# Kernel tuning notes

Measured on AMD Instinct MI355X. Metric: run time of the kernel, lower is better.

## Reference

```python
import jax, jax.numpy as jnp
import numpy as np

B, N, C, CS, CP, H, L = 1, 2048, 128, 128, 16, 4, 3
NQ, NK = 32, 128  # local attention window: n_queries, n_keys
EPS = 1e-5


def _make_beta(n):
    l = np.arange(n)[:, None]
    m = np.arange(n)[None, :]
    con = np.zeros((n, n), dtype=bool)
    for c in np.arange(NQ / 2, n, NQ):
        con |= (np.abs(l - c) < NQ / 2) & (np.abs(m - c) < NK / 2)
    return np.where(con, 0.0, -1e10).astype(np.float32)


def setup_inputs() -> dict:
    key = jax.random.key(0)
    ks = iter(jax.random.split(key, 32))
    w = lambda *shape: jax.random.normal(next(ks), shape, dtype=jnp.float32) * 0.02
    inp = {
        'a': jax.random.normal(next(ks), (B, N, C), dtype=jnp.float32),
        's': jax.random.normal(next(ks), (B, N, CS), dtype=jnp.float32),
        'z': jax.random.normal(next(ks), (B, N, N, CP), dtype=jnp.float32),
        'beta': jnp.asarray(_make_beta(N))[None],
        'ada1_ln_w': jnp.ones((L, CS)), 'ada1_lin_w': w(L, CS, C),
        'ada1_lin_b': jnp.zeros((L, C)), 'ada1_nb_w': w(L, CS, C),
        'lnz_w': jnp.ones((L, CP)), 'lnz_b': jnp.zeros((L, CP)),
        'zinj_w': w(L, CP, H),
        'q_w': w(L, C, C), 'q_b': jnp.zeros((L, C)),
        'k_w': w(L, C, C), 'v_w': w(L, C, C),
        'g_w': w(L, C, C), 'o_w': w(L, C, C),
        'agate_w': w(L, CS, C), 'agate_b': jnp.full((L, C), -2.0),
        'ada2_ln_w': jnp.ones((L, CS)), 'ada2_lin_w': w(L, CS, C),
        'ada2_lin_b': jnp.zeros((L, C)), 'ada2_nb_w': w(L, CS, C),
        'lin1_w': w(L, C, 2 * C), 'lin2_w': w(L, C, 2 * C), 'lin3_w': w(L, 2 * C, C),
        'tgate_w': w(L, CS, C), 'tgate_b': jnp.full((L, C), -2.0),
    }
    return inp


def _ln(x):
    mu = jnp.mean(x, axis=-1, keepdims=True)
    var = jnp.var(x, axis=-1, keepdims=True)
    return (x - mu) * jax.lax.rsqrt(var + EPS)


def _adaln(a, s, ln_w, lin_w, lin_b, nb_w):
    # AdaLN: LN(a) gated & shifted by LN(s)
    a = _ln(a)
    sn = _ln(s) * ln_w
    return jax.nn.sigmoid(sn @ lin_w + lin_b) * a + sn @ nb_w


def _forward(a, s, z, beta, ada1_ln_w, ada1_lin_w, ada1_lin_b, ada1_nb_w,
             lnz_w, lnz_b, zinj_w, q_w, q_b, k_w, v_w, g_w, o_w,
             agate_w, agate_b, ada2_ln_w, ada2_lin_w, ada2_lin_b, ada2_nb_w,
             lin1_w, lin2_w, lin3_w, tgate_w, tgate_b):
    b_, n_, c_ = a.shape
    h_ = zinj_w.shape[-1]
    d_ = c_ // h_
    scale = 1.0 / np.sqrt(d_).astype(np.float32)
    zn0 = _ln(z)  # shared pre-affine LN of pair rep
    for i in range(q_w.shape[0]):
        # --- AttentionPairBias ---
        ah = _adaln(a, s, ada1_ln_w[i], ada1_lin_w[i], ada1_lin_b[i], ada1_nb_w[i])
        zb = jnp.einsum('bijc,ch->bhij', zn0 * lnz_w[i] + lnz_b[i], zinj_w[i])
        q = ((ah @ q_w[i] + q_b[i]) * scale).reshape(b_, n_, h_, d_)
        k = (ah @ k_w[i]).reshape(b_, n_, h_, d_)
        v = (ah @ v_w[i]).reshape(b_, n_, h_, d_)
        scores = jnp.einsum('bihd,bjhd->bhij', q, k) + zb + beta[:, None]
        p = jax.nn.softmax(scores, axis=-1)
        o = jnp.einsum('bhij,bjhd->bihd', p, v).reshape(b_, n_, c_)
        o = o * jax.nn.sigmoid(ah @ g_w[i])
        attn = (o @ o_w[i]) * jax.nn.sigmoid(s @ agate_w[i] + agate_b[i])
        # --- ConditionedTransitionBlock ---
        th = _adaln(a, s, ada2_ln_w[i], ada2_lin_w[i], ada2_lin_b[i], ada2_nb_w[i])
        bb = jax.nn.silu(th @ lin1_w[i]) * (th @ lin2_w[i])
        trans = jax.nn.sigmoid(s @ tgate_w[i] + tgate_b[i]) * th * (bb @ lin3_w[i])
        a = attn + trans
    return a


def reference(a, s, z, beta, ada1_ln_w, ada1_lin_w, ada1_lin_b, ada1_nb_w,
              lnz_w, lnz_b, zinj_w, q_w, q_b, k_w, v_w, g_w, o_w,
              agate_w, agate_b, ada2_ln_w, ada2_lin_w, ada2_lin_b, ada2_nb_w,
              lin1_w, lin2_w, lin3_w, tgate_w, tgate_b):
    return _forward(a, s, z, beta, ada1_ln_w, ada1_lin_w, ada1_lin_b, ada1_nb_w,
                    lnz_w, lnz_b, zinj_w, q_w, q_b, k_w, v_w, g_w, o_w,
                    agate_w, agate_b, ada2_ln_w, ada2_lin_w, ada2_lin_b, ada2_nb_w,
                    lin1_w, lin2_w, lin3_w, tgate_w, tgate_b)
```

## Files before the change

### kernel.cpp

```cpp
#include <hip/hip_runtime.h>


#define NT 2048

__device__ __forceinline__ float sig_(float x) { return 1.0f / (1.0f + __expf(-x)); }

__device__ __forceinline__ float redsum32(float v) {
#pragma unroll
  for (int o = 16; o > 0; o >>= 1) v += __shfl_xor(v, o);
  return v;
}

__device__ __forceinline__ void mm4(const float* __restrict__ W, int ldw,
                                    const float* As_row, int K, int c0, float* acc) {
  const float* __restrict__ wp = W + c0;
  for (int k = 0; k < K; k += 4) {
    float4 a4 = *(const float4*)(As_row + k);
#pragma unroll
    for (int kk = 0; kk < 4; ++kk) {
      float a = ((const float*)&a4)[kk];
      float4 w0 = *(const float4*)(wp);
      acc[0] = fmaf(a, w0.x, acc[0]);
      acc[1] = fmaf(a, w0.y, acc[1]);
      acc[2] = fmaf(a, w0.z, acc[2]);
      acc[3] = fmaf(a, w0.w, acc[3]);
      wp += ldw;
    }
  }
}

__device__ __forceinline__ void mm4x2(const float* __restrict__ W1,
                                      const float* __restrict__ W2, int ldw,
                                      const float* As_row, int K, int c0,
                                      float* acc1, float* acc2) {
  const float* __restrict__ wp1 = W1 + c0;
  const float* __restrict__ wp2 = W2 + c0;
  for (int k = 0; k < K; k += 4) {
    float4 a4 = *(const float4*)(As_row + k);
#pragma unroll
    for (int kk = 0; kk < 4; ++kk) {
      float a = ((const float*)&a4)[kk];
      float4 w0 = *(const float4*)(wp1);
      float4 u0 = *(const float4*)(wp2);
      acc1[0] = fmaf(a, w0.x, acc1[0]);
      acc1[1] = fmaf(a, w0.y, acc1[1]);
      acc1[2] = fmaf(a, w0.z, acc1[2]);
      acc1[3] = fmaf(a, w0.w, acc1[3]);
      acc2[0] = fmaf(a, u0.x, acc2[0]);
      acc2[1] = fmaf(a, u0.y, acc2[1]);
      acc2[2] = fmaf(a, u0.z, acc2[2]);
      acc2[3] = fmaf(a, u0.w, acc2[3]);
      wp1 += ldw; wp2 += ldw;
    }
  }
}

__global__ __launch_bounds__(256) void k_ln_rows(const float* __restrict__ X,
                                                 float* __restrict__ Y) {
  int row  = blockIdx.x * 4 + (threadIdx.x >> 6);
  int lane = threadIdx.x & 63;
  const float* xr = X + (size_t)row * 128;
  float x0 = xr[lane], x1 = xr[lane + 64];
  float s = x0 + x1;
#pragma unroll
  for (int o = 32; o > 0; o >>= 1) s += __shfl_xor(s, o);
  float mu = s * (1.0f / 128.0f);
  float d0 = x0 - mu, d1 = x1 - mu;
  float v = d0 * d0 + d1 * d1;
#pragma unroll
  for (int o = 32; o > 0; o >>= 1) v += __shfl_xor(v, o);
  float rs = rsqrtf(v * (1.0f / 128.0f) + 1e-5f);
  float* yr = Y + (size_t)row * 128;
  yr[lane] = d0 * rs;
  yr[lane + 64] = d1 * rs;
}

__global__ __launch_bounds__(256) void k_gates(
    const float* __restrict__ s, const float* __restrict__ agw,
    const float* __restrict__ agb, const float* __restrict__ tgw,
    const float* __restrict__ tgb, float* __restrict__ gatesA,
    float* __restrict__ gatesT) {
  __shared__ float As[8 * 132];
  int r0 = blockIdx.x * 8;
  int bz = blockIdx.y;
  int l = bz % 3, which = bz / 3;
  const float* W = (which ? tgw : agw) + (size_t)l * 128 * 128;
  const float* bias = (which ? tgb : agb) + (size_t)l * 128;
  float* outp = (which ? gatesT : gatesA) + (size_t)l * NT * 128;
  int tid = threadIdx.x;
  int r = tid >> 5, sub = tid & 31;
  *(float4*)&As[r * 132 + sub * 4] =
      *(const float4*)(s + (size_t)(r0 + r) * 128 + sub * 4);
  __syncthreads();
  int c0 = sub << 2;
  float acc[4] = {0, 0, 0, 0};
  mm4(W, 128, &As[r * 132], 128, c0, acc);
  size_t base = (size_t)(r0 + r) * 128 + c0;
#pragma unroll
  for (int j = 0; j < 4; ++j) outp[base + j] = sig_(acc[j] + bias[c0 + j]);
}

__global__ __launch_bounds__(256) void k_adaln12(
    const float* __restrict__ a, const float* __restrict__ ln_s,
    const float* __restrict__ lnw1, const float* __restrict__ linw1,
    const float* __restrict__ linb1, const float* __restrict__ nbw1,
    const float* __restrict__ lnw2, const float* __restrict__ linw2,
    const float* __restrict__ linb2, const float* __restrict__ nbw2,
    float* __restrict__ ah, float* __restrict__ th) {
  __shared__ float Sn[8 * 132];
  __shared__ float La[8 * 132];
  int r0 = blockIdx.x * 8;
  int y = blockIdx.y;
  const float* lnw  = y ? lnw2 : lnw1;
  const float* linw = y ? linw2 : linw1;
  const float* linb = y ? linb2 : linb1;
  const float* nbw  = y ? nbw2 : nbw1;
  float* outp = y ? th : ah;
  int tid = threadIdx.x;
  int r = tid >> 5, sub = tid & 31;
  {
    float4 v = *(const float4*)(ln_s + (size_t)(r0 + r) * 128 + sub * 4);
    float4 sc = *(const float4*)(lnw + sub * 4);
    v.x *= sc.x; v.y *= sc.y; v.z *= sc.z; v.w *= sc.w;
    *(float4*)&Sn[r * 132 + sub * 4] = v;
  }
  {
    float4 x = *(const float4*)(a + (size_t)(r0 + r) * 128 + sub * 4);
    float s = redsum32(x.x + x.y + x.z + x.w);
    float mu = s * (1.0f / 128.0f);
    float4 d = make_float4(x.x - mu, x.y - mu, x.z - mu, x.w - mu);
    float v = redsum32(d.x * d.x + d.y * d.y + d.z * d.z + d.w * d.w);
    float rs = rsqrtf(v * (1.0f / 128.0f) + 1e-5f);
    d.x *= rs; d.y *= rs; d.z *= rs; d.w *= rs;
    *(float4*)&La[r * 132 + sub * 4] = d;
  }
  __syncthreads();
  int c0 = sub << 2;
  float acc1[4] = {0, 0, 0, 0}, acc2[4] = {0, 0, 0, 0};
  mm4x2(linw, nbw, 128, &Sn[r * 132], 128, c0, acc1, acc2);
  size_t base = (size_t)(r0 + r) * 128 + c0;
#pragma unroll
  for (int j = 0; j < 4; ++j) {
    float g = sig_(acc1[j] + linb[c0 + j]);
    outp[base + j] = g * La[r * 132 + c0 + j] + acc2[j];
  }
}

__global__ __launch_bounds__(256) void k_qkvg(
    const float* __restrict__ ah, const float* __restrict__ qw,
    const float* __restrict__ kw, const float* __restrict__ vw,
    const float* __restrict__ gw, const float* __restrict__ qb,
    float* __restrict__ qkvg) {
  __shared__ float As[8 * 132];
  int r0 = blockIdx.x * 8;
  int mat = blockIdx.y;
  const float* W = (mat == 0) ? qw : (mat == 1) ? kw : (mat == 2) ? vw : gw;
  int tid = threadIdx.x;
  int r = tid >> 5, sub = tid & 31;
  *(float4*)&As[r * 132 + sub * 4] =
      *(const float4*)(ah + (size_t)(r0 + r) * 128 + sub * 4);
  __syncthreads();
  int c0 = sub << 2;
  float acc[4] = {0, 0, 0, 0};
  mm4(W, 128, &As[r * 132], 128, c0, acc);
  float* op = qkvg + (size_t)(r0 + r) * 512 + mat * 128 + c0;
  if (mat == 0) {
#pragma unroll
    for (int j = 0; j < 4; ++j)
      op[j] = (acc[j] + qb[c0 + j]) * 0.17677669529663687f;
  } else if (mat == 3) {
#pragma unroll
    for (int j = 0; j < 4; ++j) op[j] = sig_(acc[j]);
  } else {
#pragma unroll
    for (int j = 0; j < 4; ++j) op[j] = acc[j];
  }
}

__global__ __launch_bounds__(256) void k_wattn(
    const float* __restrict__ qkvg, const float* __restrict__ z,
    const float* __restrict__ lnzw, const float* __restrict__ lnzb,
    const float* __restrict__ zinj, float* __restrict__ og,
    float* __restrict__ colpart) {
  __shared__ float Qs[8][128];
  __shared__ float S[8][4][132];
  __shared__ float KV[32][128];
  __shared__ float wz[4][16];
  __shared__ float bzw[2][4];
  __shared__ float red[2][128];

  const int tid = threadIdx.x;
  const int bx = blockIdx.x;
  if (bx >= 256) {
    int b = bx - 256;
    int rr = tid >> 7, c = tid & 127;
    float acc = 0.0f;
    for (int t = 0; t < 16; ++t) {
      int row = b * 32 + rr + t * 2;
      acc += qkvg[(size_t)row * 512 + 256 + c];
    }
    red[rr][c] = acc;
    __syncthreads();
    if (rr == 0) colpart[b * 128 + c] = red[0][c] + red[1][c];
    return;
  }

  const int win = bx >> 2, sub4 = bx & 3;
  const int cen = 16 + 32 * win;
  const int i0 = cen - 15 + 8 * sub4;
  const int nrows = (sub4 == 3) ? 7 : 8;
  const int jlo = max(0, cen - 63), jhi = min(2047, cen + 63);
  const int nk = jhi - jlo + 1;

  if (tid < 64) {
    int h = tid & 3, c = tid >> 2;
    wz[h][c] = lnzw[c] * zinj[c * 4 + h];
  }
  if (tid < 8) {
    int h = tid & 3, which = tid >> 2;
    float acc = 0.0f;
    for (int c = 0; c < 16; ++c) acc += (which ? lnzb[c] : lnzw[c]) * zinj[c * 4 + h];
    bzw[which][h] = acc;
  }
  {
    int r = tid >> 5, sub = tid & 31;
    int i = i0 + min(r, nrows - 1);
    *(float4*)&Qs[r][sub * 4] = *(const float4*)(qkvg + (size_t)i * 512 + sub * 4);
  }
  __syncthreads();

  for (int idx = tid; idx < 8 * 128; idx += 256) {
    int r = idx >> 7, jj = idx & 127;
    if (jj < nk) {
      int i = i0 + min(r, nrows - 1);
      int j = jlo + jj;
      const float* zp = z + ((size_t)i * 2048 + j) * 16;
      float x[16];
      *(float4*)&x[0]  = *(const float4*)(zp + 0);
      *(float4*)&x[4]  = *(const float4*)(zp + 4);
      *(float4*)&x[8]  = *(const float4*)(zp + 8);
      *(float4*)&x[12] = *(const float4*)(zp + 12);
      float sm = 0.0f;
#pragma unroll
      for (int c = 0; c < 16; ++c) sm += x[c];
      float mu = sm * (1.0f / 16.0f);
      float var = 0.0f;
#pragma unroll
      for (int c = 0; c < 16; ++c) { float d = x[c] - mu; var = fmaf(d, d, var); }
      float rs = rsqrtf(var * (1.0f / 16.0f) + 1e-5f);
#pragma unroll
      for (int h = 0; h < 4; ++h) {
        float dot = 0.0f;
#pragma unroll
        for (int c = 0; c < 16; ++c) dot = fmaf(x[c], wz[h][c], dot);
        S[r][h][jj] = fmaf(rs, dot - mu * bzw[0][h], bzw[1][h]);
      }
    } else {
#pragma unroll
      for (int h = 0; h < 4; ++h) S[r][h][jj] = -1e30f;
    }
  }
  __syncthreads();

  {
    const int r = tid >> 5, h = (tid >> 3) & 3, part = tid & 7;
    float qreg[32];
#pragma unroll
    for (int d4 = 0; d4 < 32; d4 += 4)
      *(float4*)&qreg[d4] = *(const float4*)&Qs[r][h * 32 + d4];
    for (int kb = 0; kb < 128; kb += 32) {
      for (int idx = tid; idx < 32 * 32; idx += 256) {
        int kk = idx >> 5, c4 = (idx & 31) << 2;
        int j = jlo + kb + kk;
        int cs = (c4 + ((kk >> 3) << 2)) & 127;
        float4 val = make_float4(0.f, 0.f, 0.f, 0.f);
        if (j <= jhi) val = *(const float4*)(qkvg + (size_t)j * 512 + 128 + c4);
        *(float4*)&KV[kk][cs] = val;
      }
      __syncthreads();
#pragma unroll
      for (int u = 0; u < 4; ++u) {
        int jj = part + (u << 3);
        int rot = (jj >> 3) << 2;
        float dot = 0.0f;
#pragma unroll
        for (int d4 = 0; d4 < 32; d4 += 4) {
          int cs = (h * 32 + d4 + rot) & 127;
          float4 kv = *(const float4*)&KV[jj][cs];
          dot = fmaf(qreg[d4 + 0], kv.x, dot);
          dot = fmaf(qreg[d4 + 1], kv.y, dot);
          dot = fmaf(qreg[d4 + 2], kv.z, dot);
          dot = fmaf(qreg[d4 + 3], kv.w, dot);
        }
        S[r][h][kb + jj] += dot;
      }
      __syncthreads();
    }
  }

  {
    const int rh = tid >> 3, part = tid & 7;
    const int sr = rh >> 2, sh = rh & 3;
    float* Srow = &S[sr][sh][0];
    float m = -1e30f;
#pragma unroll
    for (int st = 0; st < 16; ++st) m = fmaxf(m, Srow[part + (st << 3)]);
#pragma unroll
    for (int o = 4; o > 0; o >>= 1) m = fmaxf(m, __shfl_xor(m, o));
    float ss = 0.0f;
#pragma unroll
    for (int st = 0; st < 16; ++st) {
      int jj = part + (st << 3);
      float e = __expf(Srow[jj] - m);
      Srow[jj] = e;
      ss += e;
    }
#pragma unroll
    for (int o = 4; o > 0; o >>= 1) ss += __shfl_xor(ss, o);
    float inv = 1.0f / ss;
#pragma unroll
    for (int st = 0; st < 16; ++st) Srow[part + (st << 3)] *= inv;
  }
  __syncthreads();

  {
    const int r = tid >> 5, cg = tid & 31;
    const int ca = cg << 2;
    const int h = cg >> 3;
    float acc[4] = {0, 0, 0, 0};
    for (int kb = 0; kb < 128; kb += 32) {
      for (int idx = tid; idx < 32 * 32; idx += 256) {
        int kk = idx >> 5, c4 = (idx & 31) << 2;
        int j = jlo + kb + kk;
        int cs = (c4 + ((kk >> 3) << 2)) & 127;
        float4 val = make_float4(0.f, 0.f, 0.f, 0.f);
        if (j <= jhi) val = *(const float4*)(qkvg + (size_t)j * 512 + 256 + c4);
        *(float4*)&KV[kk][cs] = val;
      }
      __syncthreads();
#pragma unroll 4
      for (int kk = 0; kk < 32; ++kk) {
        int rot = (kk >> 3) << 2;
        float sa = S[r][h][kb + kk];
        float4 va = *(const float4*)&KV[kk][(ca + rot) & 127];
        acc[0] = fmaf(sa, va.x, acc[0]);
        acc[1] = fmaf(sa, va.y, acc[1]);
        acc[2] = fmaf(sa, va.z, acc[2]);
        acc[3] = fmaf(sa, va.w, acc[3]);
      }
      __syncthreads();
    }
    if (r < nrows) {
      int i = i0 + r;
      float4 ga = *(const float4*)(qkvg + (size_t)i * 512 + 384 + ca);
      float4 oa = make_float4(acc[0] * ga.x, acc[1] * ga.y, acc[2] * ga.z, acc[3] * ga.w);
      *(float4*)(og + (size_t)i * 128 + ca) = oa;
    }
  }
}

__global__ __launch_bounds__(256) void k_oproj(const float* __restrict__ og,
                                               const float* __restrict__ ow,
                                               const float* __restrict__ gA,
                                               const float* __restrict__ colpart,
                                               const float* __restrict__ qkvg,
                                               float* __restrict__ attn) {
  __shared__ float As[8 * 132];
  __shared__ float red[2][128];
  int r0 = blockIdx.x * 8;
  int tid = threadIdx.x;
  int r = tid >> 5, sub = tid & 31;
  *(float4*)&As[r * 132 + sub * 4] =
      *(const float4*)(og + (size_t)(r0 + r) * 128 + sub * 4);
  __syncthreads();
  if ((r0 & 31) == 0) {
    int col = tid & 127, half = tid >> 7;
    float acc = 0.0f;
    for (int b = half; b < 64; b += 2) acc += colpart[b * 128 + col];
    red[half][col] = acc;
    __syncthreads();
    if (half == 0) {
      float mv = (red[0][col] + red[1][col]) * (1.0f / 2048.0f);
      As[col] = mv * qkvg[(size_t)r0 * 512 + 384 + col];
    }
    __syncthreads();
  }
  int c0 = sub << 2;
  float acc[4] = {0, 0, 0, 0};
  mm4(ow, 128, &As[r * 132], 128, c0, acc);
  size_t base = (size_t)(r0 + r) * 128 + c0;
#pragma unroll
  for (int j = 0; j < 4; ++j) attn[base + j] = acc[j] * gA[base + j];
}

__global__ __launch_bounds__(256) void k_lin12(const float* __restrict__ th,
                                               const float* __restrict__ w1,
                                               const float* __restrict__ w2,
                                               float* __restrict__ bb) {
  __shared__ float As[8 * 132];
  int r0 = blockIdx.x * 8;
  int cb0 = blockIdx.y * 128;
  int tid = threadIdx.x;
  int r = tid >> 5, sub = tid & 31;
  *(float4*)&As[r * 132 + sub * 4] =
      *(const float4*)(th + (size_t)(r0 + r) * 128 + sub * 4);
  __syncthreads();
  int c0 = cb0 + (sub << 2);
  float acc1[4] = {0, 0, 0, 0}, acc2[4] = {0, 0, 0, 0};
  mm4x2(w1, w2, 256, &As[r * 132], 128, c0, acc1, acc2);
  size_t base = (size_t)(r0 + r) * 256 + c0;
#pragma unroll
  for (int j = 0; j < 4; ++j) {
    float x1 = acc1[j];
    bb[base + j] = x1 * sig_(x1) * acc2[j];
  }
}

__global__ __launch_bounds__(256) void k_lin3comb(
    const float* __restrict__ bb, const float* __restrict__ w3,
    const float* __restrict__ attn, const float* __restrict__ gT,
    const float* __restrict__ th, float* __restrict__ outp) {
  __shared__ float As[8 * 260];
  int r0 = blockIdx.x * 8;
  int tid = threadIdx.x;
  for (int idx = tid; idx < 8 * 64; idx += 256) {
    int row = idx >> 6, c4 = (idx & 63) << 2;
    *(float4*)&As[row * 260 + c4] = *(const float4*)(bb + (size_t)(r0 + row) * 256 + c4);
  }
  __syncthreads();
  int r = tid >> 5, sub = tid & 31;
  int c0 = sub << 2;
  float acc[4] = {0, 0, 0, 0};
  mm4(w3, 128, &As[r * 260], 256, c0, acc);
  size_t base = (size_t)(r0 + r) * 128 + c0;
#pragma unroll
  for (int j = 0; j < 4; ++j)
    outp[base + j] = attn[base + j] + gT[base + j] * th[base + j] * acc[j];
}

extern "C" void kernel_launch(void* const* d_in, const int* in_sizes, int n_in,
                              void* d_out, int out_size, void* d_ws, size_t ws_size,
                              hipStream_t stream) {
  (void)in_sizes; (void)n_in; (void)out_size; (void)ws_size;
  const float* A_in   = (const float*)d_in[0];
  const float* S_in   = (const float*)d_in[1];
  const float* Z_in   = (const float*)d_in[2];
  const float* ada1_ln_w  = (const float*)d_in[4];
  const float* ada1_lin_w = (const float*)d_in[5];
  const float* ada1_lin_b = (const float*)d_in[6];
  const float* ada1_nb_w  = (const float*)d_in[7];
  const float* lnz_w      = (const float*)d_in[8];
  const float* lnz_b      = (const float*)d_in[9];
  const float* zinj_w     = (const float*)d_in[10];
  const float* q_w        = (const float*)d_in[11];
  const float* q_b        = (const float*)d_in[12];
  const float* k_w        = (const float*)d_in[13];
  const float* v_w        = (const float*)d_in[14];
  const float* g_w        = (const float*)d_in[15];
  const float* o_w        = (const float*)d_in[16];
  const float* agate_w    = (const float*)d_in[17];
  const float* agate_b    = (const float*)d_in[18];
  const float* ada2_ln_w  = (const float*)d_in[19];
  const float* ada2_lin_w = (const float*)d_in[20];
  const float* ada2_lin_b = (const float*)d_in[21];
  const float* ada2_nb_w  = (const float*)d_in[22];
  const float* lin1_w     = (const float*)d_in[23];
  const float* lin2_w     = (const float*)d_in[24];
  const float* lin3_w     = (const float*)d_in[25];
  const float* tgate_w    = (const float*)d_in[26];
  const float* tgate_b    = (const float*)d_in[27];

  const int N = NT, C = 128;
  float* ws = (float*)d_ws;
  float* ln_s    = ws;
  float* ah      = ln_s + (size_t)N * C;
  float* th      = ah + (size_t)N * C;
  float* qkvg    = th + (size_t)N * C;
  float* og      = qkvg + (size_t)N * 512;
  float* attn    = og + (size_t)N * C;
  float* bb      = attn + (size_t)N * C;
  float* gatesA  = bb + (size_t)N * 256;
  float* gatesT  = gatesA + (size_t)3 * N * C;
  float* colpart = gatesT + (size_t)3 * N * C;

  dim3 blk(256);
  k_ln_rows<<<512, blk, 0, stream>>>(S_in, ln_s);
  k_gates<<<dim3(256, 6), blk, 0, stream>>>(S_in, agate_w, agate_b, tgate_w,
                                            tgate_b, gatesA, gatesT);
  const float* acur = A_in;
  for (int l = 0; l < 3; ++l) {
    k_adaln12<<<dim3(256, 2), blk, 0, stream>>>(
        acur, ln_s, ada1_ln_w + (size_t)l * C, ada1_lin_w + (size_t)l * C * C,
        ada1_lin_b + (size_t)l * C, ada1_nb_w + (size_t)l * C * C,
        ada2_ln_w + (size_t)l * C, ada2_lin_w + (size_t)l * C * C,
        ada2_lin_b + (size_t)l * C, ada2_nb_w + (size_t)l * C * C, ah, th);
    k_qkvg<<<dim3(256, 4), blk, 0, stream>>>(ah, q_w + (size_t)l * C * C,
                                             k_w + (size_t)l * C * C,
                                             v_w + (size_t)l * C * C,
                                             g_w + (size_t)l * C * C,
                                             q_b + (size_t)l * C, qkvg);
    k_lin12<<<dim3(256, 2), blk, 0, stream>>>(th, lin1_w + (size_t)l * C * 2 * C,
                                              lin2_w + (size_t)l * C * 2 * C, bb);
    k_wattn<<<320, blk, 0, stream>>>(qkvg, Z_in, lnz_w + (size_t)l * 16,
                                     lnz_b + (size_t)l * 16,
                                     zinj_w + (size_t)l * 64, og, colpart);
    k_oproj<<<256, blk, 0, stream>>>(og, o_w + (size_t)l * C * C,
                                     gatesA + (size_t)l * N * C, colpart, qkvg,
                                     attn);
    k_lin3comb<<<256, blk, 0, stream>>>(bb, lin3_w + (size_t)l * 2 * C * C, attn,
                                        gatesT + (size_t)l * N * C, th,
                                        (float*)d_out);
    acur = (const float*)d_out;
  }
}
```

Baseline: 780.6 us.

## Precompute z-bias once for all layers, prefetch K/V, fuse oproj with lin3

Adds a k_zbias kernel that reads the windowed z once and computes the layer-norm plus head projection for all three layers up front, so each layer's attention kernel loads a compact per-window bias instead of re-reading and normalising z. The attention kernel now prefetches K/V tiles into registers to overlap global loads with compute, and folds softmax normalisation into the output scaling, which removes one pass and one barrier. The output projection and lin3 combine are merged into a single tail kernel, removing the attn intermediate buffer and one launch per layer. The cost is an extra workspace buffer for the bias and more register pressure in the attention kernel.

```diff
diff --git a/kernel.cpp b/kernel.cpp
--- a/kernel.cpp
+++ b/kernel.cpp
@@ -98,6 +98,67 @@
   size_t base = (size_t)(r0 + r) * 128 + c0;
 #pragma unroll
   for (int j = 0; j < 4; ++j) outp[base + j] = sig_(acc[j] + bias[c0 + j]);
+}
+
+__global__ __launch_bounds__(256) void k_zbias(
+    const float* __restrict__ z, const float* __restrict__ lnzw,
+    const float* __restrict__ lnzb, const float* __restrict__ zinj,
+    float* __restrict__ zb) {
+  __shared__ float wz[3][4][16];
+  __shared__ float bzw[3][2][4];
+  const int tid = threadIdx.x;
+  const int bx = blockIdx.x;
+  const int win = bx >> 2, q = bx & 3;
+  const int cen = 16 + 32 * win;
+  const int i0 = cen - 15 + 8 * q;
+  const int nrows = (q == 3) ? 7 : 8;
+  const int jlo = max(0, cen - 63), jhi = min(2047, cen + 63);
+  const int nk = jhi - jlo + 1;
+  if (tid < 192) {
+    int l = tid / 64, rem = tid & 63, h = rem & 3, c = rem >> 2;
+    wz[l][h][c] = lnzw[l * 16 + c] * zinj[l * 64 + c * 4 + h];
+  }
+  if (tid < 24) {
+    int l = tid / 8, rem = tid & 7, h = rem & 3, which = rem >> 2;
+    const float* wv = (which ? lnzb : lnzw) + l * 16;
+    float acc = 0.0f;
+    for (int c = 0; c < 16; ++c) acc += wv[c] * zinj[l * 64 + c * 4 + h];
+    bzw[l][which][h] = acc;
+  }
+  __syncthreads();
+  for (int idx = tid; idx < 8 * 128; idx += 256) {
+    int r = idx >> 7, jj = idx & 127;
+    if (jj >= nk || r >= nrows) continue;
+    int i = i0 + r;
+    int j = jlo + jj;
+    const float* zp = z + ((size_t)i * 2048 + j) * 16;
+    float x[16];
+    *(float4*)&x[0]  = *(const float4*)(zp + 0);
+    *(float4*)&x[4]  = *(const float4*)(zp + 4);
+    *(float4*)&x[8]  = *(const float4*)(zp + 8);
+    *(float4*)&x[12] = *(const float4*)(zp + 12);
+    float sm = 0.0f;
+#pragma unroll
+    for (int c = 0; c < 16; ++c) sm += x[c];
+    float mu = sm * (1.0f / 16.0f);
+    float var = 0.0f;
+#pragma unroll
+    for (int c = 0; c < 16; ++c) { float d = x[c] - mu; var = fmaf(d, d, var); }
+    float rs = rsqrtf(var * (1.0f / 16.0f) + 1e-5f);
+    float* op = zb + (size_t)i * 512 + (size_t)jj * 4;
+#pragma unroll
+    for (int l = 0; l < 3; ++l) {
+      float4 o4;
+#pragma unroll
+      for (int h = 0; h < 4; ++h) {
+        float dot = 0.0f;
+#pragma unroll
+        for (int c = 0; c < 16; ++c) dot = fmaf(x[c], wz[l][h][c], dot);
+        ((float*)&o4)[h] = fmaf(rs, dot - mu * bzw[l][0][h], bzw[l][1][h]);
+      }
+      *(float4*)(op + (size_t)l * 2048 * 512) = o4;
+    }
+  }
 }
 
 __global__ __launch_bounds__(256) void k_adaln12(
@@ -178,15 +239,12 @@
 }
 
 __global__ __launch_bounds__(256) void k_wattn(
-    const float* __restrict__ qkvg, const float* __restrict__ z,
-    const float* __restrict__ lnzw, const float* __restrict__ lnzb,
-    const float* __restrict__ zinj, float* __restrict__ og,
-    float* __restrict__ colpart) {
+    const float* __restrict__ qkvg, const float* __restrict__ zb,
+    float* __restrict__ og, float* __restrict__ colpart) {
   __shared__ float Qs[8][128];
   __shared__ float S[8][4][132];
   __shared__ float KV[32][128];
-  __shared__ float wz[4][16];
-  __shared__ float bzw[2][4];
+  __shared__ float invS[8][4];
   __shared__ float red[2][128];
 
   const int tid = threadIdx.x;
@@ -212,49 +270,35 @@
   const int jlo = max(0, cen - 63), jhi = min(2047, cen + 63);
   const int nk = jhi - jlo + 1;
 
-  if (tid < 64) {
-    int h = tid & 3, c = tid >> 2;
-    wz[h][c] = lnzw[c] * zinj[c * 4 + h];
-  }
-  if (tid < 8) {
-    int h = tid & 3, which = tid >> 2;
-    float acc = 0.0f;
-    for (int c = 0; c < 16; ++c) acc += (which ? lnzb[c] : lnzw[c]) * zinj[c * 4 + h];
-    bzw[which][h] = acc;
-  }
+  int pkk[4], pc[4];
+#pragma unroll
+  for (int u = 0; u < 4; ++u) {
+    int idx = tid + u * 256;
+    pkk[u] = idx >> 5;
+    pc[u] = (idx & 31) << 2;
+  }
+  float4 pref[4];
+#pragma unroll
+  for (int u = 0; u < 4; ++u) {
+    int j = jlo + pkk[u];
+    pref[u] = (j <= jhi) ? *(const float4*)(qkvg + (size_t)j * 512 + 128 + pc[u])
+                         : make_float4(0.f, 0.f, 0.f, 0.f);
+  }
+
   {
     int r = tid >> 5, sub = tid & 31;
     int i = i0 + min(r, nrows - 1);
     *(float4*)&Qs[r][sub * 4] = *(const float4*)(qkvg + (size_t)i * 512 + sub * 4);
   }
-  __syncthreads();
-
   for (int idx = tid; idx < 8 * 128; idx += 256) {
     int r = idx >> 7, jj = idx & 127;
     if (jj < nk) {
       int i = i0 + min(r, nrows - 1);
-      int j = jlo + jj;
-      const float* zp = z + ((size_t)i * 2048 + j) * 16;
-      float x[16];
-      *(float4*)&x[0]  = *(const float4*)(zp + 0);
-      *(float4*)&x[4]  = *(const float4*)(zp + 4);
-      *(float4*)&x[8]  = *(const float4*)(zp + 8);
-      *(float4*)&x[12] = *(const float4*)(zp + 12);
-      float sm = 0.0f;
-#pragma unroll
-      for (int c = 0; c < 16; ++c) sm += x[c];
-      float mu = sm * (1.0f / 16.0f);
-      float var = 0.0f;
-#pragma unroll
-      for (int c = 0; c < 16; ++c) { float d = x[c] - mu; var = fmaf(d, d, var); }
-      float rs = rsqrtf(var * (1.0f / 16.0f) + 1e-5f);
-#pragma unroll
-      for (int h = 0; h < 4; ++h) {
-        float dot = 0.0f;
-#pragma unroll
-        for (int c = 0; c < 16; ++c) dot = fmaf(x[c], wz[h][c], dot);
-        S[r][h][jj] = fmaf(rs, dot - mu * bzw[0][h], bzw[1][h]);
-      }
+      float4 zv = *(const float4*)(zb + (size_t)i * 512 + (size_t)jj * 4);
+      S[r][0][jj] = zv.x;
+      S[r][1][jj] = zv.y;
+      S[r][2][jj] = zv.z;
+      S[r][3][jj] = zv.w;
     } else {
 #pragma unroll
       for (int h = 0; h < 4; ++h) S[r][h][jj] = -1e30f;
@@ -269,13 +313,19 @@
     for (int d4 = 0; d4 < 32; d4 += 4)
       *(float4*)&qreg[d4] = *(const float4*)&Qs[r][h * 32 + d4];
     for (int kb = 0; kb < 128; kb += 32) {
-      for (int idx = tid; idx < 32 * 32; idx += 256) {
-        int kk = idx >> 5, c4 = (idx & 31) << 2;
-        int j = jlo + kb + kk;
-        int cs = (c4 + ((kk >> 3) << 2)) & 127;
-        float4 val = make_float4(0.f, 0.f, 0.f, 0.f);
-        if (j <= jhi) val = *(const float4*)(qkvg + (size_t)j * 512 + 128 + c4);
-        *(float4*)&KV[kk][cs] = val;
+#pragma unroll
+      for (int u = 0; u < 4; ++u)
+        *(float4*)&KV[pkk[u]][(pc[u] + ((pkk[u] >> 3) << 2)) & 127] = pref[u];
+      {
+        int nxt_off = (kb < 96) ? 128 : 256;
+        int nxt_kb = (kb < 96) ? kb + 32 : 0;
+#pragma unroll
+        for (int u = 0; u < 4; ++u) {
+          int j = jlo + nxt_kb + pkk[u];
+          pref[u] = (j <= jhi)
+                        ? *(const float4*)(qkvg + (size_t)j * 512 + nxt_off + pc[u])
+                        : make_float4(0.f, 0.f, 0.f, 0.f);
+        }
       }
       __syncthreads();
 #pragma unroll
@@ -317,11 +367,8 @@
     }
 #pragma unroll
     for (int o = 4; o > 0; o >>= 1) ss += __shfl_xor(ss, o);
-    float inv = 1.0f / ss;
-#pragma unroll
-    for (int st = 0; st < 16; ++st) Srow[part + (st << 3)] *= inv;
-  }
-  __syncthreads();
+    if (part == 0) invS[sr][sh] = 1.0f / ss;
+  }
 
   {
     const int r = tid >> 5, cg = tid & 31;
@@ -329,13 +376,17 @@
     const int h = cg >> 3;
     float acc[4] = {0, 0, 0, 0};
     for (int kb = 0; kb < 128; kb += 32) {
-      for (int idx = tid; idx < 32 * 32; idx += 256) {
-        int kk = idx >> 5, c4 = (idx & 31) << 2;
-        int j = jlo + kb + kk;
-        int cs = (c4 + ((kk >> 3) << 2)) & 127;
-        float4 val = make_float4(0.f, 0.f, 0.f, 0.f);
-        if (j <= jhi) val = *(const float4*)(qkvg + (size_t)j * 512 + 256 + c4);
-        *(float4*)&KV[kk][cs] = val;
+#pragma unroll
+      for (int u = 0; u < 4; ++u)
+        *(float4*)&KV[pkk[u]][(pc[u] + ((pkk[u] >> 3) << 2)) & 127] = pref[u];
+      if (kb < 96) {
+#pragma unroll
+        for (int u = 0; u < 4; ++u) {
+          int j = jlo + kb + 32 + pkk[u];
+          pref[u] = (j <= jhi)
+                        ? *(const float4*)(qkvg + (size_t)j * 512 + 256 + pc[u])
+                        : make_float4(0.f, 0.f, 0.f, 0.f);
+        }
       }
       __syncthreads();
 #pragma unroll 4
@@ -352,45 +403,13 @@
     }
     if (r < nrows) {
       int i = i0 + r;
+      float inv = invS[r][h];
       float4 ga = *(const float4*)(qkvg + (size_t)i * 512 + 384 + ca);
-      float4 oa = make_float4(acc[0] * ga.x, acc[1] * ga.y, acc[2] * ga.z, acc[3] * ga.w);
+      float4 oa = make_float4(acc[0] * inv * ga.x, acc[1] * inv * ga.y,
+                              acc[2] * inv * ga.z, acc[3] * inv * ga.w);
       *(float4*)(og + (size_t)i * 128 + ca) = oa;
     }
   }
-}
-
-__global__ __launch_bounds__(256) void k_oproj(const float* __restrict__ og,
-                                               const float* __restrict__ ow,
-                                               const float* __restrict__ gA,
-                                               const float* __restrict__ colpart,
-                                               const float* __restrict__ qkvg,
-                                               float* __restrict__ attn) {
-  __shared__ float As[8 * 132];
-  __shared__ float red[2][128];
-  int r0 = blockIdx.x * 8;
-  int tid = threadIdx.x;
-  int r = tid >> 5, sub = tid & 31;
-  *(float4*)&As[r * 132 + sub * 4] =
-      *(const float4*)(og + (size_t)(r0 + r) * 128 + sub * 4);
-  __syncthreads();
-  if ((r0 & 31) == 0) {
-    int col = tid & 127, half = tid >> 7;
-    float acc = 0.0f;
-    for (int b = half; b < 64; b += 2) acc += colpart[b * 128 + col];
-    red[half][col] = acc;
-    __syncthreads();
-    if (half == 0) {
-      float mv = (red[0][col] + red[1][col]) * (1.0f / 2048.0f);
-      As[col] = mv * qkvg[(size_t)r0 * 512 + 384 + col];
-    }
-    __syncthreads();
-  }
-  int c0 = sub << 2;
-  float acc[4] = {0, 0, 0, 0};
-  mm4(ow, 128, &As[r * 132], 128, c0, acc);
-  size_t base = (size_t)(r0 + r) * 128 + c0;
-#pragma unroll
-  for (int j = 0; j < 4; ++j) attn[base + j] = acc[j] * gA[base + j];
 }
 
 __global__ __launch_bounds__(256) void k_lin12(const float* __restrict__ th,
@@ -416,26 +435,49 @@
   }
 }
 
-__global__ __launch_bounds__(256) void k_lin3comb(
-    const float* __restrict__ bb, const float* __restrict__ w3,
-    const float* __restrict__ attn, const float* __restrict__ gT,
+__global__ __launch_bounds__(256) void k_tail(
+    const float* __restrict__ og, const float* __restrict__ ow,
+    const float* __restrict__ gA, const float* __restrict__ colpart,
+    const float* __restrict__ qkvg, const float* __restrict__ bbuf,
+    const float* __restrict__ w3, const float* __restrict__ gT,
     const float* __restrict__ th, float* __restrict__ outp) {
-  __shared__ float As[8 * 260];
+  __shared__ float Ao[8 * 132];
+  __shared__ float Bb[8 * 260];
+  __shared__ float red[2][128];
   int r0 = blockIdx.x * 8;
   int tid = threadIdx.x;
+  int r = tid >> 5, sub = tid & 31;
+  *(float4*)&Ao[r * 132 + sub * 4] =
+      *(const float4*)(og + (size_t)(r0 + r) * 128 + sub * 4);
   for (int idx = tid; idx < 8 * 64; idx += 256) {
     int row = idx >> 6, c4 = (idx & 63) << 2;
-    *(float4*)&As[row * 260 + c4] = *(const float4*)(bb + (size_t)(r0 + row) * 256 + c4);
-  }
-  __syncthreads();
-  int r = tid >> 5, sub = tid & 31;
+    *(float4*)&Bb[row * 260 + c4] =
+        *(const float4*)(bbuf + (size_t)(r0 + row) * 256 + c4);
+  }
+  __syncthreads();
+  if ((r0 & 31) == 0) {
+    int col = tid & 127, half = tid >> 7;
+    float acc = 0.0f;
+    for (int b = half; b < 64; b += 2) acc += colpart[b * 128 + col];
+    red[half][col] = acc;
+    __syncthreads();
+    if (half == 0) {
+      float mv = (red[0][col] + red[1][col]) * (1.0f / 2048.0f);
+      Ao[col] = mv * qkvg[(size_t)r0 * 512 + 384 + col];
+    }
+    __syncthreads();
+  }
   int c0 = sub << 2;
-  float acc[4] = {0, 0, 0, 0};
-  mm4(w3, 128, &As[r * 260], 256, c0, acc);
+  float acc1[4] = {0, 0, 0, 0};
+  mm4(ow, 128, &Ao[r * 132], 128, c0, acc1);
+  float acc3[4] = {0, 0, 0, 0};
+  mm4(w3, 128, &Bb[r * 260], 256, c0, acc3);
   size_t base = (size_t)(r0 + r) * 128 + c0;
 #pragma unroll
-  for (int j = 0; j < 4; ++j)
-    outp[base + j] = attn[base + j] + gT[base + j] * th[base + j] * acc[j];
+  for (int j = 0; j < 4; ++j) {
+    float attnv = acc1[j] * gA[base + j];
+    outp[base + j] = attnv + gT[base + j] * th[base + j] * acc3[j];
+  }
 }
 
 extern "C" void kernel_launch(void* const* d_in, const int* in_sizes, int n_in,
@@ -477,16 +519,17 @@
   float* th      = ah + (size_t)N * C;
   float* qkvg    = th + (size_t)N * C;
   float* og      = qkvg + (size_t)N * 512;
-  float* attn    = og + (size_t)N * C;
-  float* bb      = attn + (size_t)N * C;
+  float* bb      = og + (size_t)N * C;
   float* gatesA  = bb + (size_t)N * 256;
   float* gatesT  = gatesA + (size_t)3 * N * C;
   float* colpart = gatesT + (size_t)3 * N * C;
+  float* zb      = colpart + (size_t)64 * 128;
 
   dim3 blk(256);
   k_ln_rows<<<512, blk, 0, stream>>>(S_in, ln_s);
   k_gates<<<dim3(256, 6), blk, 0, stream>>>(S_in, agate_w, agate_b, tgate_w,
                                             tgate_b, gatesA, gatesT);
+  k_zbias<<<256, blk, 0, stream>>>(Z_in, lnz_w, lnz_b, zinj_w, zb);
   const float* acur = A_in;
   for (int l = 0; l < 3; ++l) {
     k_adaln12<<<dim3(256, 2), blk, 0, stream>>>(
@@ -501,15 +544,11 @@
                                              q_b + (size_t)l * C, qkvg);
     k_lin12<<<dim3(256, 2), blk, 0, stream>>>(th, lin1_w + (size_t)l * C * 2 * C,
                                               lin2_w + (size_t)l * C * 2 * C, bb);
-    k_wattn<<<320, blk, 0, stream>>>(qkvg, Z_in, lnz_w + (size_t)l * 16,
-                                     lnz_b + (size_t)l * 16,
-                                     zinj_w + (size_t)l * 64, og, colpart);
-    k_oproj<<<256, blk, 0, stream>>>(og, o_w + (size_t)l * C * C,
-                                     gatesA + (size_t)l * N * C, colpart, qkvg,
-                                     attn);
-    k_lin3comb<<<256, blk, 0, stream>>>(bb, lin3_w + (size_t)l * 2 * C * C, attn,
-                                        gatesT + (size_t)l * N * C, th,
-                                        (float*)d_out);
+    k_wattn<<<320, blk, 0, stream>>>(qkvg, zb + (size_t)l * N * 512, og, colpart);
+    k_tail<<<256, blk, 0, stream>>>(og, o_w + (size_t)l * C * C,
+                                    gatesA + (size_t)l * N * C, colpart, qkvg, bb,
+                                    lin3_w + (size_t)l * 2 * C * C,
+                                    gatesT + (size_t)l * N * C, th, (float*)d_out);
     acur = (const float*)d_out;
   }
 }
```

After: 860.8 us. 1.1x slower.
